# Performance work log

Measured on AMD Instinct MI355X. Metric: run time of the kernel, lower is better.

## Reference

```python
import jax, jax.numpy as jnp
import numpy as np

G, N, DEG = 64, 2048, 8          # graphs, nodes/graph, avg degree
NTOT = G * N                      # 131072 nodes
E = NTOT * DEG                    # 1048576 edges
K = int(np.ceil(0.2 * N))         # 410 nodes kept per graph (SAGPooling ratio=0.2)
NK = G * K                        # 26240 pooled nodes
H, C = 3, 20                      # GAT heads, per-head channels
NEG_BIG = jnp.float32(-1e30)


def gcn(x, src, dst, W, b, n):
    """PyG GCNConv: x' = D^-1/2 (A+I) D^-1/2 x W + b (edge weight 1)."""
    h = x @ W
    deg = jax.ops.segment_sum(jnp.ones(src.shape[0], x.dtype), dst, num_segments=n) + 1.0
    dinv = jax.lax.rsqrt(deg)
    coef = dinv[src] * dinv[dst]                    # [E]
    agg = jax.ops.segment_sum(h[src] * coef[:, None], dst, num_segments=n)
    agg = agg + h * (dinv * dinv)[:, None]          # self loops
    return agg + b


def setup_inputs() -> dict:
    key = jax.random.key(0)
    ks = jax.random.split(key, 16)
    # edges constrained within each graph: per-graph local indices + offsets
    off = jnp.repeat(jnp.arange(G, dtype=jnp.int32) * N, N * DEG)   # [E]
    src = jax.random.randint(ks[0], (E,), 0, N, dtype=jnp.int32) + off
    dst = jax.random.randint(ks[1], (E,), 0, N, dtype=jnp.int32) + off
    batch = jnp.repeat(jnp.arange(G, dtype=jnp.int32), N)           # [NTOT]
    x = jax.random.normal(ks[2], (NTOT, 5), jnp.float32)
    s = 0.1
    return {
        "x": x, "src": src, "dst": dst, "batch": batch,
        "W1": jax.random.normal(ks[3], (5, 10)) * s,   "b1": jnp.zeros((10,)),
        "Ws": jax.random.normal(ks[4], (10, 1)) * s,   "bs": jnp.zeros((1,)),
        "Wg": jax.random.normal(ks[5], (10, H * C)) * s,
        "a_src": jax.random.normal(ks[6], (H, C)) * s,
        "a_dst": jax.random.normal(ks[7], (H, C)) * s,
        "bg": jnp.zeros((H * C,)),
        "Wf1": jax.random.normal(ks[8], (60, 30)) * s, "bf1": jnp.zeros((30,)),
        "Wf2": jax.random.normal(ks[9], (30, 3)) * s,  "bf2": jnp.zeros((3,)),
    }


def reference(x, src, dst, batch, W1, b1, Ws, bs, Wg, a_src, a_dst, bg, Wf1, bf1, Wf2, bf2):
    n = x.shape[0]
    # GCNConv(5,10)
    x1 = gcn(x, src, dst, W1, b1, n)                              # [NTOT,10]
    # SAGPooling: GCN scorer, top-k per graph, gate by tanh(score)
    score = gcn(x1, src, dst, Ws, bs, n)[:, 0]                    # [NTOT]
    _, topi = jax.lax.top_k(score.reshape(G, N), K)               # [G,K]
    perm = (topi + (jnp.arange(G) * N)[:, None]).reshape(-1)      # [NK] global ids
    xp = x1[perm] * jnp.tanh(score[perm])[:, None]                # [NK,10]
    # remap edges; drop (mask) edges touching removed nodes (filter_adj)
    new_idx = jnp.full((n,), -1, jnp.int32).at[perm].set(jnp.arange(NK, dtype=jnp.int32))
    s2, d2 = new_idx[src], new_idx[dst]
    emask = (s2 >= 0) & (d2 >= 0)
    s2 = jnp.where(emask, s2, 0)
    d2 = jnp.where(emask, d2, 0)
    # GATConv(10, 20, heads=3) with self loops
    h = (xp @ Wg).reshape(NK, H, C)
    al_s = jnp.sum(h * a_src, -1)                                 # [NK,H]
    al_d = jnp.sum(h * a_dst, -1)
    loop = jnp.arange(NK, dtype=jnp.int32)
    sa = jnp.concatenate([s2, loop])
    da = jnp.concatenate([d2, loop])
    ma = jnp.concatenate([emask, jnp.ones((NK,), bool)])
    logits = jax.nn.leaky_relu(al_s[sa] + al_d[da], 0.2)          # [E+NK,H]
    logits = jnp.where(ma[:, None], logits, NEG_BIG)
    mx = jax.ops.segment_max(logits, da, num_segments=NK)         # finite: self loops
    w = jnp.exp(logits - mx[da]) * ma[:, None]
    denom = jax.ops.segment_sum(w, da, num_segments=NK)
    alpha = w / denom[da]                                         # edge softmax
    out = jax.ops.segment_sum(h[sa] * alpha[..., None], da, num_segments=NK)  # [NK,H,C]
    xg = out.reshape(NK, H * C) + bg                              # concat heads -> 60
    # scatter_add readout over graphs
    g = jax.ops.segment_sum(xg, batch[perm], num_segments=G)      # [G,60]
    # MLP + LogSoftmax
    z = jax.nn.relu(g @ Wf1 + bf1) @ Wf2 + bf2                    # [G,3]
    return jax.nn.log_softmax(z, axis=1)
```

## Files before the change

### kernel.cpp

```cpp
#include <hip/hip_runtime.h>
#include <math.h>

#define G    64
#define NPG  2048
#define NTOT (G * NPG)
#define EPG  (NPG * 8)
#define KSEL 410
#define NH   3
#define NC   20
#define HC   60
#define FCAP 24
#define KPAD 512
#define RP   12

#define OFF_H1P   0
#define OFF_XP    0
#define OFF_WRED2 0
#define OFF_FADJ  16400
#define OFF_FCNT  36080
#define OFF_HF    37728
#define OFF_CSR   98304
#define OFF_HIST  131072
#define OFF_RS    139264
#define OFF_ALS   139264
#define OFF_ALD   144184
#define OFF_SK    147456
#define OFF_GOUT  151024
#define OFF_HID   151264
#define OFF_NEWL  155648
#define OFF_PERML 159744
#define OFF_WSUM  160568
#define OFF_FLAGS 160632
#define ARENA_SZ  160648

__device__ inline float leaky(float x) { return x >= 0.f ? x : 0.2f * x; }

__device__ inline int wave_incl_scan(int v) {
    int lane = threadIdx.x & 63;
#pragma unroll
    for (int d = 1; d < 64; d <<= 1) {
        int t = __shfl_up(v, d, 64);
        if (lane >= d) v += t;
    }
    return v;
}

__global__ __launch_bounds__(1024, 4) void k_all(
    const float* __restrict__ x, const int* __restrict__ src, const int* __restrict__ dst,
    const float* __restrict__ W1, const float* __restrict__ b1,
    const float* __restrict__ Ws, const float* __restrict__ bs,
    const float* __restrict__ Wg, const float* __restrict__ a_srcw,
    const float* __restrict__ a_dstw, const float* __restrict__ bg,
    const float* __restrict__ Wf1, const float* __restrict__ bf1,
    const float* __restrict__ Wf2, const float* __restrict__ bf2,
    float* __restrict__ out)
{
    __shared__ __align__(16) char arena[ARENA_SZ];
    float*          h1p   = (float*)(arena + OFF_H1P);
    float*          xpL   = (float*)(arena + OFF_XP);
    float*          wred2 = (float*)(arena + OFF_WRED2);
    unsigned short* fadjL = (unsigned short*)(arena + OFF_FADJ);
    int*            fcntL = (int*)(arena + OFF_FCNT);
    float*          hfL   = (float*)(arena + OFF_HF);
    unsigned short* csrL  = (unsigned short*)(arena + OFF_CSR);
    int*            hist  = (int*)(arena + OFF_HIST);
    float*          prB   = (float*)(arena + OFF_HIST);
    int*            rsL   = (int*)(arena + OFF_RS);
    float*          alsL  = (float*)(arena + OFF_ALS);
    float*          aldL  = (float*)(arena + OFF_ALD);
    unsigned*       skL   = (unsigned*)(arena + OFF_SK);
    float*          goutL = (float*)(arena + OFF_GOUT);
    float*          hidL  = (float*)(arena + OFF_HID);
    unsigned short* newLs = (unsigned short*)(arena + OFF_NEWL);
    unsigned short* permL = (unsigned short*)(arena + OFF_PERML);
    int*            wsumL = (int*)(arena + OFF_WSUM);
    int*            flags = (int*)(arena + OFF_FLAGS);
#define bselS  flags[0]
#define bneedS flags[1]

    int g = blockIdx.x, tid = threadIdx.x, wid = tid >> 6;
    int nbase = g * NPG, ebase = g * EPG;

    for (int i = tid; i < NPG; i += 1024) hist[i] = 0;
    for (int i = tid; i < NPG; i += 1024) {
        const float* xr = x + (size_t)(nbase + i) * 5;
        float x0 = xr[0], x1v = xr[1], x2 = xr[2], x3 = xr[3], x4 = xr[4];
        float4* row = (float4*)(h1p + i * RP);
        row[0] = make_float4(x0, x1v, x2, x3);
        row[1] = make_float4(x4, 0.f, 0.f, 0.f);
    }
    __syncthreads();
    for (int e = tid; e < EPG; e += 1024)
        atomicAdd(&hist[dst[ebase + e] - nbase], 1);
    __syncthreads();
    {
        int b2 = tid * 2;
        int v0 = hist[b2], v1 = hist[b2 + 1];
        int s = v0 + v1;
        int incl = wave_incl_scan(s);
        if ((tid & 63) == 63) wsumL[wid] = incl;
        __syncthreads();
        int pre = 0;
#pragma unroll
        for (int w = 0; w < 16; w++) { int t = wsumL[w]; if (w < wid) pre += t; }
        int base = pre + incl - s;
        rsL[b2] = base;
        rsL[b2 + 1] = base + v0;
        float di0 = rsqrtf((float)v0 + 1.0f);
        float di1 = rsqrtf((float)v1 + 1.0f);
        h1p[b2 * RP + 5]        = di0;
        h1p[b2 * RP + 10]       = di0;
        h1p[(b2 + 1) * RP + 5]  = di1;
        h1p[(b2 + 1) * RP + 10] = di1;
        hist[b2] = 0; hist[b2 + 1] = 0;
    }
    __syncthreads();
    for (int e = tid; e < EPG; e += 1024) {
        int ee = ebase + e;
        int sl = src[ee] - nbase;
        int dl = dst[ee] - nbase;
        int pos = rsL[dl] + atomicAdd(&hist[dl], 1);
        csrL[pos] = (unsigned short)sl;
    }
    __syncthreads();

    {
        int i0 = tid, i1 = tid + 1024;
        int e0 = rsL[i0], e0e = rsL[i0 + 1];
        int e1 = rsL[i1], e1e = (i1 == NPG - 1) ? EPG : rsL[i1 + 1];
        float a0[5], a1[5];
#pragma unroll
        for (int j = 0; j < 5; j++) { a0[j] = 0.f; a1[j] = 0.f; }
        while (e0 < e0e || e1 < e1e) {
            if (e0 < e0e) {
                int s = csrL[e0++];
                float4 r0 = *(const float4*)(h1p + s * RP);
                float2 r1 = *(const float2*)(h1p + s * RP + 4);
                float dv = r1.y;
                a0[0] += r0.x * dv; a0[1] += r0.y * dv; a0[2] += r0.z * dv;
                a0[3] += r0.w * dv; a0[4] += r1.x * dv;
            }
            if (e1 < e1e) {
                int s = csrL[e1++];
                float4 r0 = *(const float4*)(h1p + s * RP);
                float2 r1 = *(const float2*)(h1p + s * RP + 4);
                float dv = r1.y;
                a1[0] += r0.x * dv; a1[1] += r0.y * dv; a1[2] += r0.z * dv;
                a1[3] += r0.w * dv; a1[4] += r1.x * dv;
            }
        }
        float4 s0 = *(const float4*)(h1p + i0 * RP);
        float2 s0b = *(const float2*)(h1p + i0 * RP + 4);
        float4 s1 = *(const float4*)(h1p + i1 * RP);
        float2 s1b = *(const float2*)(h1p + i1 * RP + 4);
        float di0 = s0b.y, d20 = di0 * di0;
        float di1 = s1b.y, d21 = di1 * di1;
        float y0[5], y1[5];
        y0[0] = a0[0] * di0 + s0.x * d20;
        y0[1] = a0[1] * di0 + s0.y * d20;
        y0[2] = a0[2] * di0 + s0.z * d20;
        y0[3] = a0[3] * di0 + s0.w * d20;
        y0[4] = a0[4] * di0 + s0b.x * d20;
        y1[0] = a1[0] * di1 + s1.x * d21;
        y1[1] = a1[1] * di1 + s1.y * d21;
        y1[2] = a1[2] * di1 + s1.z * d21;
        y1[3] = a1[3] * di1 + s1.w * d21;
        y1[4] = a1[4] * di1 + s1b.x * d21;
        float v0[10], v1[10];
#pragma unroll
        for (int k = 0; k < 10; k++) {
            float b = b1[k];
            float c0 = b, c1 = b;
#pragma unroll
            for (int j = 0; j < 5; j++) {
                float w = W1[j * 10 + k];
                c0 += y0[j] * w;
                c1 += y1[j] * w;
            }
            v0[k] = c0; v1[k] = c1;
        }
        float hs0 = 0.f, hs1 = 0.f;
#pragma unroll
        for (int k = 0; k < 10; k++) { float w = Ws[k]; hs0 += v0[k] * w; hs1 += v1[k] * w; }
        __syncthreads();
        float4* w0 = (float4*)(h1p + i0 * RP);
        w0[0] = make_float4(v0[0], v0[1], v0[2], v0[3]);
        w0[1] = make_float4(v0[4], v0[5], v0[6], v0[7]);
        w0[2] = make_float4(v0[8], v0[9], di0, hs0);
        float4* w1 = (float4*)(h1p + i1 * RP);
        w1[0] = make_float4(v1[0], v1[1], v1[2], v1[3]);
        w1[1] = make_float4(v1[4], v1[5], v1[6], v1[7]);
        w1[2] = make_float4(v1[8], v1[9], di1, hs1);
        prB[i0] = hs0 * di0;
        prB[i1] = hs1 * di1;
    }
    __syncthreads();

    {
        float bsv = bs[0];
        int i0 = tid, i1 = tid + 1024;
        float2 own0 = *(const float2*)(h1p + i0 * RP + 10);
        float2 own1 = *(const float2*)(h1p + i1 * RP + 10);
        int e0 = rsL[i0], e0e = rsL[i0 + 1];
        int e1 = rsL[i1], e1e = (i1 == NPG - 1) ? EPG : rsL[i1 + 1];
        float a0 = 0.f, a1 = 0.f;
        while (e0 < e0e || e1 < e1e) {
            if (e0 < e0e) a0 += prB[csrL[e0++]];
            if (e1 < e1e) a1 += prB[csrL[e1++]];
        }
        float sc0 = own0.x * a0 + own0.y * own0.x * own0.x + bsv;
        float sc1 = own1.x * a1 + own1.y * own1.x * own1.x + bsv;
        unsigned u0 = __float_as_uint(sc0);
        unsigned u1 = __float_as_uint(sc1);
        skL[i0] = (u0 & 0x80000000u) ? ~u0 : (u0 | 0x80000000u);
        skL[i1] = (u1 & 0x80000000u) ? ~u1 : (u1 | 0x80000000u);
        newLs[i0] = 0xFFFFu; newLs[i1] = 0xFFFFu;
    }
    int need = KSEL;
    unsigned prefix = 0;
    __syncthreads();
    for (int i = tid; i < NPG; i += 1024) hist[i] = 0;
    __syncthreads();

    for (int lv = 0; lv < 3; lv++) {
        for (int i = tid; i < NPG; i += 1024) {
            unsigned k = skL[i];
            bool match; unsigned bb;
            if (lv == 0)      { match = true;                  bb = k >> 21; }
            else if (lv == 1) { match = ((k >> 21) == prefix); bb = (k >> 10) & 0x7FFu; }
            else              { match = ((k >> 10) == prefix); bb = k & 0x3FFu; }
            if (match) atomicAdd(&hist[bb], 1);
        }
        __syncthreads();
        int b2 = tid * 2;
        int v0 = hist[b2], v1 = hist[b2 + 1];
        hist[b2] = 0; hist[b2 + 1] = 0;
        int s = v0 + v1;
        int incl = wave_incl_scan(s);
        if ((tid & 63) == 63) wsumL[wid] = incl;
        __syncthreads();
        int pre = 0, tot = 0;
#pragma unroll
        for (int w = 0; w < 16; w++) { int t = wsumL[w]; if (w < wid) pre += t; tot += t; }
        int base = pre + incl - s;
        { int Sb = tot - base;        int Sb1 = Sb - v0; if (Sb >= need && Sb1 < need) { bselS = b2;     bneedS = need - Sb1; } }
        { int Sb = tot - (base + v0); int Sb1 = Sb - v1; if (Sb >= need && Sb1 < need) { bselS = b2 + 1; bneedS = need - Sb1; } }
        __syncthreads();
        if (lv == 0)      prefix = (unsigned)bselS;
        else if (lv == 1) prefix = (prefix << 11) | (unsigned)bselS;
        else              prefix = (prefix << 10) | (unsigned)bselS;
        need = bneedS;
    }
    unsigned T = prefix;
    int greaterCnt = KSEL - need;

    {
        int b2 = tid * 2;
        unsigned k0 = skL[b2], k1 = skL[b2 + 1];
        int gt0 = k0 > T ? 1 : 0, gt1 = k1 > T ? 1 : 0;
        int eq0 = k0 == T ? 1 : 0, eq1 = k1 == T ? 1 : 0;
        int pack = ((gt0 + gt1) << 16) | (eq0 + eq1);
        int incl = wave_incl_scan(pack);
        if ((tid & 63) == 63) wsumL[wid] = incl;
        __syncthreads();
        int pre = 0;
#pragma unroll
        for (int w = 0; w < 16; w++) { int t = wsumL[w]; if (w < wid) pre += t; }
        int base = pre + incl - pack;
        int gb = base >> 16, eb = base & 0xFFFF;
        if (gt0) { permL[gb] = (unsigned short)b2; newLs[b2] = (unsigned short)gb; }
        if (gt1) { int r = gb + gt0; permL[r] = (unsigned short)(b2 + 1); newLs[b2 + 1] = (unsigned short)r; }
        if (eq0 && eb < need) { int p = greaterCnt + eb; permL[p] = (unsigned short)b2; newLs[b2] = (unsigned short)p; }
        if (eq1) { int r = eb + eq0; if (r < need) { int p = greaterCnt + r; permL[p] = (unsigned short)(b2 + 1); newLs[b2 + 1] = (unsigned short)p; } }
    }
    __syncthreads();

    {
        float4 rq0, rq1, rq2; float tt = 0.f;
        bool havep = (tid < KSEL);
        if (havep) {
            int iL = permL[tid];
            unsigned k = skL[iL];
            unsigned u = (k & 0x80000000u) ? (k & 0x7FFFFFFFu) : ~k;
            tt = tanhf(__uint_as_float(u));
            const float4* xr = (const float4*)(h1p + iL * RP);
            rq0 = xr[0]; rq1 = xr[1]; rq2 = xr[2];
        }
        __syncthreads();
        if (havep) {
            float* xp = xpL + tid * 10;
            xp[0] = rq0.x * tt; xp[1] = rq0.y * tt; xp[2] = rq0.z * tt; xp[3] = rq0.w * tt;
            xp[4] = rq1.x * tt; xp[5] = rq1.y * tt; xp[6] = rq1.z * tt; xp[7] = rq1.w * tt;
            xp[8] = rq2.x * tt; xp[9] = rq2.y * tt;
        }
    }
    __syncthreads();

    for (int p = tid; p < KSEL; p += 1024) {
        int iL = permL[p];
        int p0 = rsL[iL], p1 = (iL == NPG - 1) ? EPG : rsL[iL + 1];
        int c = 0;
        int e = p0;
        while (e < p1) {
            int n = p1 - e; n = n > 8 ? 8 : n;
            int b8[8];
#pragma unroll
            for (int j = 0; j < 8; j++) b8[j] = csrL[e + (j < n ? j : 0)];
            unsigned short n8[8];
#pragma unroll
            for (int j = 0; j < 8; j++) n8[j] = newLs[b8[j]];
#pragma unroll
            for (int j = 0; j < 8; j++)
                if (j < n && n8[j] != 0xFFFFu && c < FCAP) fadjL[p * FCAP + c++] = n8[j];
            e += n;
        }
        fcntL[p] = c;
    }
    __syncthreads();

    for (int rnd = 0; rnd < 2; rnd++) {
        int task = rnd == 0 ? tid : 1024 + tid;
        bool on = rnd == 0 || tid < KPAD;
        if (on) {
            int hh = __builtin_amdgcn_readfirstlane(task >> 9);
            int p = task & (KPAD - 1);
            if (p < KSEL) {
                float xi[10];
#pragma unroll
                for (int k = 0; k < 10; k++) xi[k] = xpL[p * 10 + k];
                float v[NC];
                float as_ = 0.f, ad_ = 0.f;
#pragma unroll
                for (int c = 0; c < NC; c++) {
                    int j = hh * NC + c;
                    float vv = 0.f;
#pragma unroll
                    for (int k = 0; k < 10; k++) vv += xi[k] * Wg[k * HC + j];
                    v[c] = vv;
                    as_ += vv * a_srcw[j];
                    ad_ += vv * a_dstw[j];
                }
                float4* hr = (float4*)(hfL + p * HC + hh * NC);
#pragma unroll
                for (int q = 0; q < 5; q++)
                    hr[q] = make_float4(v[4 * q], v[4 * q + 1], v[4 * q + 2], v[4 * q + 3]);
                alsL[p * NH + hh] = as_;
                aldL[p * NH + hh] = ad_;
            }
        }
    }
    __syncthreads();

    {
        float res[NC];
#pragma unroll
        for (int rnd = 0; rnd < 2; rnd++) {
            int task = rnd == 0 ? tid : 1024 + tid;
            bool on = rnd == 0 || tid < KPAD;
            int hh = task >> 9, p = task & (KPAD - 1);
            if (on) {
                if (p < KSEL) {
                    float aldp = aldL[p * NH + hh];
                    float lself = leaky(alsL[p * NH + hh] + aldp);
                    int c = fcntL[p];
                    const float4* hp = (const float4*)(hfL + p * HC + hh * NC);
                    float4 r0 = hp[0], r1 = hp[1], r2 = hp[2], r3 = hp[3], r4 = hp[4];
                    float wsum = 1.f;
                    for (int e = 0; e < c; e++) {
                        int idx = fadjL[p * FCAP + e];
                        float w = __expf(leaky(alsL[idx * NH + hh] + aldp) - lself);
                        wsum += w;
                        const float4* hq = (const float4*)(hfL + idx * HC + hh * NC);
                        float4 t0 = hq[0], t1 = hq[1], t2 = hq[2], t3 = hq[3], t4 = hq[4];
                        r0.x += w * t0.x; r0.y += w * t0.y; r0.z += w * t0.z; r0.w += w * t0.w;
                        r1.x += w * t1.x; r1.y += w * t1.y; r1.z += w * t1.z; r1.w += w * t1.w;
                        r2.x += w * t2.x; r2.y += w * t2.y; r2.z += w * t2.z; r2.w += w * t2.w;
                        r3.x += w * t3.x; r3.y += w * t3.y; r3.z += w * t3.z; r3.w += w * t3.w;
                        r4.x += w * t4.x; r4.y += w * t4.y; r4.z += w * t4.z; r4.w += w * t4.w;
                    }
                    float inv = 1.f / wsum;
                    res[0] = r0.x * inv;  res[1] = r0.y * inv;  res[2] = r0.z * inv;  res[3] = r0.w * inv;
                    res[4] = r1.x * inv;  res[5] = r1.y * inv;  res[6] = r1.z * inv;  res[7] = r1.w * inv;
                    res[8] = r2.x * inv;  res[9] = r2.y * inv;  res[10] = r2.z * inv; res[11] = r2.w * inv;
                    res[12] = r3.x * inv; res[13] = r3.y * inv; res[14] = r3.z * inv; res[15] = r3.w * inv;
                    res[16] = r4.x * inv; res[17] = r4.y * inv; res[18] = r4.z * inv; res[19] = r4.w * inv;
                } else {
#pragma unroll
                    for (int cc = 0; cc < NC; cc++) res[cc] = 0.f;
                }
#pragma unroll
                for (int cc = 0; cc < NC; cc++) {
                    float v = res[cc];
                    v += __shfl_xor(v, 1, 64);
                    v += __shfl_xor(v, 2, 64);
                    v += __shfl_xor(v, 4, 64);
                    res[cc] = v;
                }
                if ((tid & 7) == 0) {
                    int slot = hh * 64 + (p >> 3);
                    float* gp = wred2 + slot * NC;
#pragma unroll
                    for (int cc = 0; cc < NC; cc++) gp[cc] = res[cc];
                }
            }
        }
    }
    __syncthreads();
    if (tid < HC) {
        int hh = tid / NC, c = tid - hh * NC;
        float a = 0.f;
        for (int w = 0; w < 64; w++) a += wred2[(hh * 64 + w) * NC + c];
        goutL[tid] = a + (float)KSEL * bg[tid];
    }
    __syncthreads();

    if (tid < 30) {
        float s = bf1[tid];
#pragma unroll
        for (int k = 0; k < HC; k++) s += goutL[k] * Wf1[k * 30 + tid];
        hidL[tid] = s > 0.f ? s : 0.f;
    }
    __syncthreads();
    if (tid == 0) {
        float z[3];
#pragma unroll
        for (int j = 0; j < 3; j++) {
            float s = bf2[j];
            for (int k = 0; k < 30; k++) s += hidL[k] * Wf2[k * 3 + j];
            z[j] = s;
        }
        float m = fmaxf(z[0], fmaxf(z[1], z[2]));
        float lse = logf(expf(z[0] - m) + expf(z[1] - m) + expf(z[2] - m)) + m;
#pragma unroll
        for (int j = 0; j < 3; j++) out[g * 3 + j] = z[j] - lse;
    }
}

extern "C" void kernel_launch(void* const* d_in, const int* in_sizes, int n_in,
                              void* d_out, int out_size, void* d_ws, size_t ws_size,
                              hipStream_t stream) {
    const float* x     = (const float*)d_in[0];
    const int*   src   = (const int*)d_in[1];
    const int*   dst   = (const int*)d_in[2];
    const float* W1    = (const float*)d_in[4];
    const float* b1    = (const float*)d_in[5];
    const float* Ws    = (const float*)d_in[6];
    const float* bs    = (const float*)d_in[7];
    const float* Wg    = (const float*)d_in[8];
    const float* a_src = (const float*)d_in[9];
    const float* a_dst = (const float*)d_in[10];
    const float* bg    = (const float*)d_in[11];
    const float* Wf1   = (const float*)d_in[12];
    const float* bf1   = (const float*)d_in[13];
    const float* Wf2   = (const float*)d_in[14];
    const float* bf2   = (const float*)d_in[15];
    float* out = (float*)d_out;
    (void)d_ws; (void)ws_size;

    k_all<<<G, 1024, 0, stream>>>(x, src, dst, W1, b1, Ws, bs, Wg, a_src, a_dst,
                                  bg, Wf1, bf1, Wf2, bf2, out);
}
```

Baseline: 129.1 us.

## Vectorize edge loads, keep radix keys in registers, fuse adjacency build, use DPP reductions

Edge index reads in the histogram and CSR-fill loops now use int4 loads, so each thread handles four edges per iteration. Radix-select keys stay in registers instead of being reread from LDS, and the pooled-adjacency build is folded into the gating block, which removes one barrier. The 8-lane shuffle reductions become DPP row operations, and the second round plus the final reduction skip padded slots past 448/52. The DPP patterns and the tightened bounds depend on exact lane layouts and on KSEL fitting inside 52 groups of 8, so a wrong mapping would silently change the result.

```diff
diff --git a/kernel.cpp b/kernel.cpp
--- a/kernel.cpp
+++ b/kernel.cpp
@@ -42,6 +42,17 @@
         int t = __shfl_up(v, d, 64);
         if (lane >= d) v += t;
     }
+    return v;
+}
+
+__device__ inline float dpp_sum8(float v) {
+    int t;
+    t = __builtin_amdgcn_update_dpp(0, __float_as_int(v), 0xB1, 0xF, 0xF, true);
+    v += __int_as_float(t);
+    t = __builtin_amdgcn_update_dpp(0, __float_as_int(v), 0x4E, 0xF, 0xF, true);
+    v += __int_as_float(t);
+    t = __builtin_amdgcn_update_dpp(0, __float_as_int(v), 0x141, 0xF, 0xF, true);
+    v += __int_as_float(t);
     return v;
 }
 
@@ -80,6 +91,8 @@
 
     int g = blockIdx.x, tid = threadIdx.x, wid = tid >> 6;
     int nbase = g * NPG, ebase = g * EPG;
+    const int4* dst4 = (const int4*)(dst + ebase);
+    const int4* src4 = (const int4*)(src + ebase);
 
     for (int i = tid; i < NPG; i += 1024) hist[i] = 0;
     for (int i = tid; i < NPG; i += 1024) {
@@ -90,8 +103,13 @@
         row[1] = make_float4(x4, 0.f, 0.f, 0.f);
     }
     __syncthreads();
-    for (int e = tid; e < EPG; e += 1024)
-        atomicAdd(&hist[dst[ebase + e] - nbase], 1);
+    for (int e4 = tid; e4 < EPG / 4; e4 += 1024) {
+        int4 d = dst4[e4];
+        atomicAdd(&hist[d.x - nbase], 1);
+        atomicAdd(&hist[d.y - nbase], 1);
+        atomicAdd(&hist[d.z - nbase], 1);
+        atomicAdd(&hist[d.w - nbase], 1);
+    }
     __syncthreads();
     {
         int b2 = tid * 2;
@@ -115,12 +133,14 @@
         hist[b2] = 0; hist[b2 + 1] = 0;
     }
     __syncthreads();
-    for (int e = tid; e < EPG; e += 1024) {
-        int ee = ebase + e;
-        int sl = src[ee] - nbase;
-        int dl = dst[ee] - nbase;
-        int pos = rsL[dl] + atomicAdd(&hist[dl], 1);
-        csrL[pos] = (unsigned short)sl;
+    for (int e4 = tid; e4 < EPG / 4; e4 += 1024) {
+        int4 s4 = src4[e4];
+        int4 d4 = dst4[e4];
+        int dl, pos;
+        dl = d4.x - nbase; pos = rsL[dl] + atomicAdd(&hist[dl], 1); csrL[pos] = (unsigned short)(s4.x - nbase);
+        dl = d4.y - nbase; pos = rsL[dl] + atomicAdd(&hist[dl], 1); csrL[pos] = (unsigned short)(s4.y - nbase);
+        dl = d4.z - nbase; pos = rsL[dl] + atomicAdd(&hist[dl], 1); csrL[pos] = (unsigned short)(s4.z - nbase);
+        dl = d4.w - nbase; pos = rsL[dl] + atomicAdd(&hist[dl], 1); csrL[pos] = (unsigned short)(s4.w - nbase);
     }
     __syncthreads();
 
@@ -196,6 +216,7 @@
     }
     __syncthreads();
 
+    unsigned kr0, kr1;
     {
         float bsv = bs[0];
         int i0 = tid, i1 = tid + 1024;
@@ -212,8 +233,10 @@
         float sc1 = own1.x * a1 + own1.y * own1.x * own1.x + bsv;
         unsigned u0 = __float_as_uint(sc0);
         unsigned u1 = __float_as_uint(sc1);
-        skL[i0] = (u0 & 0x80000000u) ? ~u0 : (u0 | 0x80000000u);
-        skL[i1] = (u1 & 0x80000000u) ? ~u1 : (u1 | 0x80000000u);
+        kr0 = (u0 & 0x80000000u) ? ~u0 : (u0 | 0x80000000u);
+        kr1 = (u1 & 0x80000000u) ? ~u1 : (u1 | 0x80000000u);
+        skL[i0] = kr0;
+        skL[i1] = kr1;
         newLs[i0] = 0xFFFFu; newLs[i1] = 0xFFFFu;
     }
     int need = KSEL;
@@ -223,8 +246,9 @@
     __syncthreads();
 
     for (int lv = 0; lv < 3; lv++) {
-        for (int i = tid; i < NPG; i += 1024) {
-            unsigned k = skL[i];
+#pragma unroll
+        for (int t = 0; t < 2; t++) {
+            unsigned k = t == 0 ? kr0 : kr1;
             bool match; unsigned bb;
             if (lv == 0)      { match = true;                  bb = k >> 21; }
             else if (lv == 1) { match = ((k >> 21) == prefix); bb = (k >> 10) & 0x7FFu; }
@@ -277,9 +301,10 @@
 
     {
         float4 rq0, rq1, rq2; float tt = 0.f;
+        int iL = 0;
         bool havep = (tid < KSEL);
         if (havep) {
-            int iL = permL[tid];
+            iL = permL[tid];
             unsigned k = skL[iL];
             unsigned u = (k & 0x80000000u) ? (k & 0x7FFFFFFFu) : ~k;
             tt = tanhf(__uint_as_float(u));
@@ -292,35 +317,30 @@
             xp[0] = rq0.x * tt; xp[1] = rq0.y * tt; xp[2] = rq0.z * tt; xp[3] = rq0.w * tt;
             xp[4] = rq1.x * tt; xp[5] = rq1.y * tt; xp[6] = rq1.z * tt; xp[7] = rq1.w * tt;
             xp[8] = rq2.x * tt; xp[9] = rq2.y * tt;
-        }
-    }
-    __syncthreads();
-
-    for (int p = tid; p < KSEL; p += 1024) {
-        int iL = permL[p];
-        int p0 = rsL[iL], p1 = (iL == NPG - 1) ? EPG : rsL[iL + 1];
-        int c = 0;
-        int e = p0;
-        while (e < p1) {
-            int n = p1 - e; n = n > 8 ? 8 : n;
-            int b8[8];
-#pragma unroll
-            for (int j = 0; j < 8; j++) b8[j] = csrL[e + (j < n ? j : 0)];
-            unsigned short n8[8];
-#pragma unroll
-            for (int j = 0; j < 8; j++) n8[j] = newLs[b8[j]];
-#pragma unroll
-            for (int j = 0; j < 8; j++)
-                if (j < n && n8[j] != 0xFFFFu && c < FCAP) fadjL[p * FCAP + c++] = n8[j];
-            e += n;
-        }
-        fcntL[p] = c;
+            int p0 = rsL[iL], p1 = (iL == NPG - 1) ? EPG : rsL[iL + 1];
+            int c = 0;
+            int e = p0;
+            while (e < p1) {
+                int n = p1 - e; n = n > 8 ? 8 : n;
+                int b8[8];
+#pragma unroll
+                for (int j = 0; j < 8; j++) b8[j] = csrL[e + (j < n ? j : 0)];
+                unsigned short n8[8];
+#pragma unroll
+                for (int j = 0; j < 8; j++) n8[j] = newLs[b8[j]];
+#pragma unroll
+                for (int j = 0; j < 8; j++)
+                    if (j < n && n8[j] != 0xFFFFu && c < FCAP) fadjL[tid * FCAP + c++] = n8[j];
+                e += n;
+            }
+            fcntL[tid] = c;
+        }
     }
     __syncthreads();
 
     for (int rnd = 0; rnd < 2; rnd++) {
         int task = rnd == 0 ? tid : 1024 + tid;
-        bool on = rnd == 0 || tid < KPAD;
+        bool on = rnd == 0 || tid < 448;
         if (on) {
             int hh = __builtin_amdgcn_readfirstlane(task >> 9);
             int p = task & (KPAD - 1);
@@ -356,7 +376,7 @@
 #pragma unroll
         for (int rnd = 0; rnd < 2; rnd++) {
             int task = rnd == 0 ? tid : 1024 + tid;
-            bool on = rnd == 0 || tid < KPAD;
+            bool on = rnd == 0 || tid < 448;
             int hh = task >> 9, p = task & (KPAD - 1);
             if (on) {
                 if (p < KSEL) {
@@ -389,13 +409,7 @@
                     for (int cc = 0; cc < NC; cc++) res[cc] = 0.f;
                 }
 #pragma unroll
-                for (int cc = 0; cc < NC; cc++) {
-                    float v = res[cc];
-                    v += __shfl_xor(v, 1, 64);
-                    v += __shfl_xor(v, 2, 64);
-                    v += __shfl_xor(v, 4, 64);
-                    res[cc] = v;
-                }
+                for (int cc = 0; cc < NC; cc++) res[cc] = dpp_sum8(res[cc]);
                 if ((tid & 7) == 0) {
                     int slot = hh * 64 + (p >> 3);
                     float* gp = wred2 + slot * NC;
@@ -409,7 +423,7 @@
     if (tid < HC) {
         int hh = tid / NC, c = tid - hh * NC;
         float a = 0.f;
-        for (int w = 0; w < 64; w++) a += wred2[(hh * 64 + w) * NC + c];
+        for (int w = 0; w < 52; w++) a += wred2[(hh * 64 + w) * NC + c];
         goutL[tid] = a + (float)KSEL * bg[tid];
     }
     __syncthreads();
```

New measurement: 119.6 us, median of 2. 1.08x faster.
